# Performance work log

Hardware: AMD Instinct MI355X
Metric: run time of the kernel (lower is better)

The kernel has to match this reference:

```python
import jax, jax.numpy as jnp
import numpy as np

POOLER_SIZE = 56
SPATIAL_SCALE = 0.25
B, P, K, H, W, A = 4, 512, 4, 200, 336, 14
IMG_H, IMG_W = H / SPATIAL_SCALE, W / SPATIAL_SCALE


def _roi_align_one(feat, boxes):
    """torchvision RoIAlign (aligned=False, sampling_ratio=1).
    feat: [K, H, W]; boxes: [P, 4] as (x1, y1, x2, y2) in image coords.
    Returns [P, K, ps, ps]."""
    Kc, Hf, Wf = feat.shape
    ps = POOLER_SIZE
    s = SPATIAL_SCALE
    x1 = boxes[:, 0] * s
    y1 = boxes[:, 1] * s
    x2 = boxes[:, 2] * s
    y2 = boxes[:, 3] * s
    rw = jnp.maximum(x2 - x1, 1.0)  # non-aligned mode clamps roi size to >= 1
    rh = jnp.maximum(y2 - y1, 1.0)
    bw = rw / ps
    bh = rh / ps
    grid = jnp.arange(ps, dtype=feat.dtype) + 0.5  # sampling_ratio=1 -> bin center
    xs = x1[:, None] + grid[None, :] * bw[:, None]  # [P, ps]
    ys = y1[:, None] + grid[None, :] * bh[:, None]  # [P, ps]
    xx = jnp.broadcast_to(xs[:, None, :], (xs.shape[0], ps, ps))  # [P, ps, ps]
    yy = jnp.broadcast_to(ys[:, :, None], (ys.shape[0], ps, ps))
    valid = (yy > -1.0) & (yy < Hf) & (xx > -1.0) & (xx < Wf)
    y = jnp.clip(yy, 0.0, Hf - 1)
    x = jnp.clip(xx, 0.0, Wf - 1)
    y0 = jnp.floor(y).astype(jnp.int32)
    x0 = jnp.floor(x).astype(jnp.int32)
    y1i = jnp.minimum(y0 + 1, Hf - 1)
    x1i = jnp.minimum(x0 + 1, Wf - 1)
    ly = y - y0
    lx = x - x0
    f = feat.reshape(Kc, Hf * Wf)

    def gather(yi, xi):
        idx = (yi * Wf + xi).reshape(-1)
        return jnp.take(f, idx, axis=1).reshape((Kc,) + yi.shape)  # [K, P, ps, ps]

    w00 = ((1.0 - ly) * (1.0 - lx))[None]
    w01 = ((1.0 - ly) * lx)[None]
    w10 = (ly * (1.0 - lx))[None]
    w11 = (ly * lx)[None]
    v = (gather(y0, x0) * w00 + gather(y0, x1i) * w01 +
         gather(y1i, x0) * w10 + gather(y1i, x1i) * w11)
    v = v * valid[None].astype(feat.dtype)
    return jnp.transpose(v, (1, 0, 2, 3))  # [P, K, ps, ps]


def _bilinear_resize_ac(x, ps):
    """F.interpolate(mode='bilinear', align_corners=True) on last two dims (square a->ps)."""
    a = x.shape[-1]
    src = jnp.arange(ps, dtype=x.dtype) * ((a - 1) / (ps - 1))
    i0 = jnp.clip(jnp.floor(src).astype(jnp.int32), 0, a - 2)
    i1 = i0 + 1
    t = src - i0.astype(x.dtype)
    rows = x[..., i0, :] * (1.0 - t)[:, None] + x[..., i1, :] * t[:, None]  # [..., ps, a]
    out = rows[..., :, i0] * (1.0 - t) + rows[..., :, i1] * t  # [..., ps, ps]
    return out


def setup_inputs() -> dict:
    key = jax.random.key(0)
    k1, k2, k3, k4, k5, k6 = jax.random.split(key, 6)
    bases = jax.random.normal(k1, (B, K, H, W), dtype=jnp.float32)
    attention_proposals = jax.random.normal(k2, (B, P, K, A, A), dtype=jnp.float32)
    # realistic boxes inside an 800x1344 image
    x1 = jax.random.uniform(k3, (B, P)) * (IMG_W - 64.0)
    y1 = jax.random.uniform(k4, (B, P)) * (IMG_H - 64.0)
    bw = 32.0 + jax.random.uniform(k5, (B, P)) * 256.0
    bh = 32.0 + jax.random.uniform(k6, (B, P)) * 256.0
    x2 = jnp.minimum(x1 + bw, IMG_W)
    y2 = jnp.minimum(y1 + bh, IMG_H)
    box_proposals = jnp.stack([x1, y1, x2, y2], axis=-1).astype(jnp.float32)  # [B, P, 4]
    return {"bases": bases, "box_proposals": box_proposals,
            "attention_proposals": attention_proposals}


def reference(bases, box_proposals, attention_proposals):
    ps = POOLER_SIZE
    rois = jax.vmap(_roi_align_one)(bases, box_proposals)  # [B, P, K, ps, ps]
    attn = _bilinear_resize_ac(attention_proposals, ps)    # [B, P, K, ps, ps]
    attn = jax.nn.softmax(attn, axis=2)                    # softmax over num_bases
    return (attn * rois).sum(axis=2)                       # [B, P, ps, ps]
```

## Files before the change

### kernel.cpp

```cpp
#include <hip/hip_runtime.h>
#include <math.h>

#define B_  4
#define P_  512
#define K_  4
#define H_  200
#define W_  336
#define A_  14
#define PS_ 56
#define SCALE_ 0.25f

__global__ __launch_bounds__(256) void blender_kernel(
    const float* __restrict__ bases,
    const float* __restrict__ boxes,
    const float* __restrict__ attn,
    float* __restrict__ out)
{
    const int bp = blockIdx.x;
    const int b  = bp / P_;

    __shared__ float tile[K_][A_ * A_];

    const float* ap = attn + (size_t)bp * (K_ * A_ * A_);
    for (int i = threadIdx.x; i < K_ * A_ * A_; i += blockDim.x) {
        tile[i / (A_ * A_)][i % (A_ * A_)] = ap[i];
    }

    const float* bx = boxes + (size_t)bp * 4;
    const float x1 = bx[0] * SCALE_;
    const float y1 = bx[1] * SCALE_;
    const float x2 = bx[2] * SCALE_;
    const float y2 = bx[3] * SCALE_;
    const float bw = fmaxf(x2 - x1, 1.0f) * (1.0f / PS_);
    const float bh = fmaxf(y2 - y1, 1.0f) * (1.0f / PS_);

    __syncthreads();

    const float* base_b = bases + (size_t)b * (K_ * H_ * W_);
    float* outp = out + (size_t)bp * (PS_ * PS_);

    const float r = (float)(A_ - 1) / (float)(PS_ - 1);

    for (int idx = threadIdx.x; idx < PS_ * PS_; idx += blockDim.x) {
        const int py = idx / PS_;
        const int px = idx % PS_;

        const float sx = x1 + (px + 0.5f) * bw;
        const float sy = y1 + (py + 0.5f) * bh;
        const bool valid = (sy > -1.0f) && (sy < (float)H_) &&
                           (sx > -1.0f) && (sx < (float)W_);
        const float cy = fminf(fmaxf(sy, 0.0f), (float)(H_ - 1));
        const float cx = fminf(fmaxf(sx, 0.0f), (float)(W_ - 1));
        const int y0 = (int)cy;
        const int x0 = (int)cx;
        const int y1i = min(y0 + 1, H_ - 1);
        const int x1i = min(x0 + 1, W_ - 1);
        const float ly = cy - (float)y0;
        const float lx = cx - (float)x0;
        const float w00 = (1.0f - ly) * (1.0f - lx);
        const float w01 = (1.0f - ly) * lx;
        const float w10 = ly * (1.0f - lx);
        const float w11 = ly * lx;
        const float vscale = valid ? 1.0f : 0.0f;

        const float srcx = (float)px * r;
        const float srcy = (float)py * r;
        int ix0 = (int)srcx; ix0 = min(ix0, A_ - 2);
        int iy0 = (int)srcy; iy0 = min(iy0, A_ - 2);
        const float tx = srcx - (float)ix0;
        const float ty = srcy - (float)iy0;
        const float a00 = (1.0f - ty) * (1.0f - tx);
        const float a01 = (1.0f - ty) * tx;
        const float a10 = ty * (1.0f - tx);
        const float a11 = ty * tx;

        float av[K_], rv[K_];
        float m = -1e30f;
        #pragma unroll
        for (int k = 0; k < K_; ++k) {
            const float* t = tile[k];
            const float a = t[iy0 * A_ + ix0]     * a00
                          + t[iy0 * A_ + ix0 + 1] * a01
                          + t[(iy0 + 1) * A_ + ix0]     * a10
                          + t[(iy0 + 1) * A_ + ix0 + 1] * a11;
            av[k] = a;
            m = fmaxf(m, a);

            const float* f = base_b + (size_t)k * (H_ * W_);
            const float v = f[y0 * W_ + x0]  * w00
                          + f[y0 * W_ + x1i] * w01
                          + f[y1i * W_ + x0]  * w10
                          + f[y1i * W_ + x1i] * w11;
            rv[k] = v * vscale;
        }

        float e[K_];
        float s = 0.0f;
        #pragma unroll
        for (int k = 0; k < K_; ++k) { e[k] = __expf(av[k] - m); s += e[k]; }
        const float inv = 1.0f / s;
        float acc = 0.0f;
        #pragma unroll
        for (int k = 0; k < K_; ++k) acc += e[k] * inv * rv[k];

        outp[idx] = acc;
    }
}

extern "C" void kernel_launch(void* const* d_in, const int* in_sizes, int n_in,
                              void* d_out, int out_size, void* d_ws, size_t ws_size,
                              hipStream_t stream) {
    const float* bases = (const float*)d_in[0];
    const float* boxes = (const float*)d_in[1];
    const float* attn  = (const float*)d_in[2];
    float* out = (float*)d_out;

    dim3 grid(B_ * P_);
    dim3 block(256);
    blender_kernel<<<grid, block, 0, stream>>>(bases, boxes, attn, out);
}
```

Before: 102.4 us.

## Precompute separable ROI and resize coefficients in shared memory, two outputs per thread

Per-column and per-row RoIAlign sample offsets and weights are computed once per block into shared tables, and the attention resize is split into a horizontal pass stored in shared memory followed by a vertical lerp per pixel. Each thread now produces two adjacent outputs written as a float2. The softmax drops the max subtraction and uses a hardware reciprocal. This removes redundant per-pixel index and weight math, but adds an extra barrier and more shared memory, and dropping the max shift risks overflow for large logits.

```diff
diff --git a/kernel.cpp b/kernel.cpp
--- a/kernel.cpp
+++ b/kernel.cpp
@@ -9,6 +9,8 @@
 #define A_  14
 #define PS_ 56
 #define SCALE_ 0.25f
+#define HWB_ (H_ * W_ * 4)
+#define NUNIT_ (PS_ * PS_ / 2)
 
 __global__ __launch_bounds__(256) void blender_kernel(
     const float* __restrict__ bases,
@@ -16,94 +18,133 @@
     const float* __restrict__ attn,
     float* __restrict__ out)
 {
-    const int bp = blockIdx.x;
-    const int b  = bp / P_;
+    const int tid = threadIdx.x;
+    const int bp  = blockIdx.x;
+    const int b   = bp / P_;
 
-    __shared__ float tile[K_][A_ * A_];
+    __shared__ float  smTile[K_ * A_ * A_];
+    __shared__ float  smR[K_ * A_ * PS_];
+    __shared__ float4 smRX[PS_];
+    __shared__ float4 smRY[PS_];
+    __shared__ float2 smAY[PS_];
 
     const float* ap = attn + (size_t)bp * (K_ * A_ * A_);
-    for (int i = threadIdx.x; i < K_ * A_ * A_; i += blockDim.x) {
-        tile[i / (A_ * A_)][i % (A_ * A_)] = ap[i];
-    }
+    for (int i = tid; i < K_ * A_ * A_; i += 256) smTile[i] = ap[i];
 
     const float* bx = boxes + (size_t)bp * 4;
-    const float x1 = bx[0] * SCALE_;
-    const float y1 = bx[1] * SCALE_;
-    const float x2 = bx[2] * SCALE_;
-    const float y2 = bx[3] * SCALE_;
-    const float bw = fmaxf(x2 - x1, 1.0f) * (1.0f / PS_);
-    const float bh = fmaxf(y2 - y1, 1.0f) * (1.0f / PS_);
+    const float rr = (float)(A_ - 1) / (float)(PS_ - 1);
+
+    if (tid < PS_) {
+        const int px = tid;
+        const float x1 = bx[0] * SCALE_;
+        const float x2 = bx[2] * SCALE_;
+        const float bw = fmaxf(x2 - x1, 1.0f) * (1.0f / PS_);
+        const float sx = x1 + (px + 0.5f) * bw;
+        const float vx = (sx > -1.0f && sx < (float)W_) ? 1.0f : 0.0f;
+        const float cx = fminf(fmaxf(sx, 0.0f), (float)(W_ - 1));
+        const int   x0 = (int)cx;
+        const int   x1i = min(x0 + 1, W_ - 1);
+        const float lx = cx - (float)x0;
+        float4 v;
+        v.x = __int_as_float(x0 * 4);
+        v.y = __int_as_float((x1i - x0) * 4);
+        v.z = lx * vx;
+        v.w = (1.0f - lx) * vx;
+        smRX[px] = v;
+    } else if (tid >= 64 && tid < 64 + PS_) {
+        const int py = tid - 64;
+        const float y1 = bx[1] * SCALE_;
+        const float y2 = bx[3] * SCALE_;
+        const float bh = fmaxf(y2 - y1, 1.0f) * (1.0f / PS_);
+        const float sy = y1 + (py + 0.5f) * bh;
+        const float vy = (sy > -1.0f && sy < (float)H_) ? 1.0f : 0.0f;
+        const float cy = fminf(fmaxf(sy, 0.0f), (float)(H_ - 1));
+        const int   y0 = (int)cy;
+        const int   y1i = min(y0 + 1, H_ - 1);
+        const float ly = cy - (float)y0;
+        float4 v;
+        v.x = __int_as_float(y0 * W_ * 4);
+        v.y = __int_as_float((y1i - y0) * W_ * 4);
+        v.z = ly * vy;
+        v.w = (1.0f - ly) * vy;
+        smRY[py] = v;
+        const float srcy = (float)py * rr;
+        int iy0 = min((int)srcy, A_ - 2);
+        float2 a;
+        a.x = __int_as_float(iy0 * PS_);
+        a.y = srcy - (float)iy0;
+        smAY[py] = a;
+    }
 
     __syncthreads();
 
-    const float* base_b = bases + (size_t)b * (K_ * H_ * W_);
+    for (int i = tid; i < K_ * A_ * PS_; i += 256) {
+        const int k  = i / (A_ * PS_);
+        const int r1 = i - k * (A_ * PS_);
+        const int ay = r1 / PS_;
+        const int px = r1 - ay * PS_;
+        const float srcx = (float)px * rr;
+        int ix0 = min((int)srcx, A_ - 2);
+        const float tx = srcx - (float)ix0;
+        const float* t = smTile + k * (A_ * A_) + ay * A_ + ix0;
+        smR[i] = t[0] * (1.0f - tx) + t[1] * tx;
+    }
+
+    __syncthreads();
+
+    const char* base_b = (const char*)(bases + (size_t)b * (K_ * H_ * W_));
     float* outp = out + (size_t)bp * (PS_ * PS_);
 
-    const float r = (float)(A_ - 1) / (float)(PS_ - 1);
+    for (int u = tid; u < NUNIT_; u += 256) {
+        const int py  = u / (PS_ / 2);
+        const int px0 = (u - py * (PS_ / 2)) * 2;
 
-    for (int idx = threadIdx.x; idx < PS_ * PS_; idx += blockDim.x) {
-        const int py = idx / PS_;
-        const int px = idx % PS_;
+        const float4 ry = smRY[py];
+        const int yoff = __float_as_int(ry.x);
+        const int dy   = __float_as_int(ry.y);
+        const float ly = ry.z, cly = ry.w;
+        const float2 ayv = smAY[py];
+        const int ayoff = __float_as_int(ayv.x);
+        const float ty = ayv.y, cty = 1.0f - ty;
 
-        const float sx = x1 + (px + 0.5f) * bw;
-        const float sy = y1 + (py + 0.5f) * bh;
-        const bool valid = (sy > -1.0f) && (sy < (float)H_) &&
-                           (sx > -1.0f) && (sx < (float)W_);
-        const float cy = fminf(fmaxf(sy, 0.0f), (float)(H_ - 1));
-        const float cx = fminf(fmaxf(sx, 0.0f), (float)(W_ - 1));
-        const int y0 = (int)cy;
-        const int x0 = (int)cx;
-        const int y1i = min(y0 + 1, H_ - 1);
-        const int x1i = min(x0 + 1, W_ - 1);
-        const float ly = cy - (float)y0;
-        const float lx = cx - (float)x0;
-        const float w00 = (1.0f - ly) * (1.0f - lx);
-        const float w01 = (1.0f - ly) * lx;
-        const float w10 = ly * (1.0f - lx);
-        const float w11 = ly * lx;
-        const float vscale = valid ? 1.0f : 0.0f;
+        float res[2];
+        #pragma unroll
+        for (int j = 0; j < 2; ++j) {
+            const int px = px0 + j;
+            const float4 rx = smRX[px];
+            const int xoff = __float_as_int(rx.x);
+            const int dx   = __float_as_int(rx.y);
+            const float lx = rx.z, clx = rx.w;
 
-        const float srcx = (float)px * r;
-        const float srcy = (float)py * r;
-        int ix0 = (int)srcx; ix0 = min(ix0, A_ - 2);
-        int iy0 = (int)srcy; iy0 = min(iy0, A_ - 2);
-        const float tx = srcx - (float)ix0;
-        const float ty = srcy - (float)iy0;
-        const float a00 = (1.0f - ty) * (1.0f - tx);
-        const float a01 = (1.0f - ty) * tx;
-        const float a10 = ty * (1.0f - tx);
-        const float a11 = ty * tx;
+            const float w00 = cly * clx, w01 = cly * lx;
+            const float w10 = ly * clx,  w11 = ly * lx;
 
-        float av[K_], rv[K_];
-        float m = -1e30f;
-        #pragma unroll
-        for (int k = 0; k < K_; ++k) {
-            const float* t = tile[k];
-            const float a = t[iy0 * A_ + ix0]     * a00
-                          + t[iy0 * A_ + ix0 + 1] * a01
-                          + t[(iy0 + 1) * A_ + ix0]     * a10
-                          + t[(iy0 + 1) * A_ + ix0 + 1] * a11;
-            av[k] = a;
-            m = fmaxf(m, a);
+            const int o00 = yoff + xoff;
+            const int o01 = o00 + dx;
+            const int o10 = o00 + dy;
+            const int o11 = o01 + dy;
 
-            const float* f = base_b + (size_t)k * (H_ * W_);
-            const float v = f[y0 * W_ + x0]  * w00
-                          + f[y0 * W_ + x1i] * w01
-                          + f[y1i * W_ + x0]  * w10
-                          + f[y1i * W_ + x1i] * w11;
-            rv[k] = v * vscale;
+            const float* rbase = smR + ayoff + px;
+
+            float s = 0.0f, acc = 0.0f;
+            #pragma unroll
+            for (int k = 0; k < K_; ++k) {
+                const char* fb = base_b + k * HWB_;
+                const float v = *(const float*)(fb + o00) * w00
+                              + *(const float*)(fb + o01) * w01
+                              + *(const float*)(fb + o10) * w10
+                              + *(const float*)(fb + o11) * w11;
+                const float a0 = rbase[k * (A_ * PS_)];
+                const float a1 = rbase[k * (A_ * PS_) + PS_];
+                const float a  = a0 * cty + a1 * ty;
+                const float e  = __expf(a);
+                s   += e;
+                acc += e * v;
+            }
+            res[j] = acc * __builtin_amdgcn_rcpf(s);
         }
-
-        float e[K_];
-        float s = 0.0f;
-        #pragma unroll
-        for (int k = 0; k < K_; ++k) { e[k] = __expf(av[k] - m); s += e[k]; }
-        const float inv = 1.0f / s;
-        float acc = 0.0f;
-        #pragma unroll
-        for (int k = 0; k < K_; ++k) acc += e[k] * inv * rv[k];
-
-        outp[idx] = acc;
+        float2 st; st.x = res[0]; st.y = res[1];
+        *(float2*)(outp + py * PS_ + px0) = st;
     }
 }
 
@@ -115,7 +156,5 @@
     const float* attn  = (const float*)d_in[2];
     float* out = (float*)d_out;
 
-    dim3 grid(B_ * P_);
-    dim3 block(256);
-    blender_kernel<<<grid, block, 0, stream>>>(bases, boxes, attn, out);
+    blender_kernel<<<dim3(B_ * P_), dim3(256), 0, stream>>>(bases, boxes, attn, out);
 }
```

New measurement: 119.6 us. +16.8%, slower.
